# Optimization experiments

Hardware: AMD Instinct MI355X
Metric: run time of the kernel (lower is better)

## Reference

```python
import jax, jax.numpy as jnp
import numpy as np

N_SRC, N_DST, N_EDGE, D_IN, D_HID, D_OUT = 100000, 25000, 300000, 256, 256, 256


def setup_inputs() -> dict:
    key = jax.random.key(0)
    ks = jax.random.split(key, 9)
    # forward tensor args
    h_src = jax.random.normal(ks[0], (N_SRC, D_IN), dtype=jnp.float32)
    h_dst = jax.random.normal(ks[1], (N_DST, D_IN), dtype=jnp.float32)
    weights = jax.random.uniform(ks[2], (N_EDGE,), dtype=jnp.float32)
    src_idx = jax.random.randint(ks[3], (N_EDGE,), 0, N_SRC)
    dst_idx = jax.random.randint(ks[4], (N_EDGE,), 0, N_DST)
    # learned parameters (xavier_uniform with relu gain, zero bias)
    gain = float(np.sqrt(2.0))
    def xavier(k, fan_in, fan_out):
        a = gain * np.sqrt(6.0 / (fan_in + fan_out))
        return jax.random.uniform(k, (fan_in, fan_out), dtype=jnp.float32, minval=-a, maxval=a)
    Q_w = xavier(ks[5], D_IN, D_HID)            # stored [in, out]
    Q_b = jnp.zeros((D_HID,), dtype=jnp.float32)
    W_w = xavier(ks[6], D_IN + D_HID, D_OUT)    # stored [in, out]
    W_b = jnp.zeros((D_OUT,), dtype=jnp.float32)
    return {"h_src": h_src, "h_dst": h_dst, "weights": weights,
            "Q_w": Q_w, "Q_b": Q_b, "W_w": W_w, "W_b": W_b,
            "src_idx": src_idx, "dst_idx": dst_idx}


def reference(h_src, h_dst, weights, Q_w, Q_b, W_w, W_b, src_idx, dst_idx):
    n_dst = h_dst.shape[0]
    # nft = relu(Q(h_src))  (dropout is eval-mode identity)
    nft = jax.nn.relu(h_src @ Q_w + Q_b)                     # [N_src, H]
    # weighted neighbor sum: u_mul_e + sum over edges per dst node
    msg = nft[src_idx] * weights[:, None]                    # [E, H]
    n = jax.ops.segment_sum(msg, dst_idx, num_segments=n_dst)          # [N_dst, H]
    ws = jax.ops.segment_sum(weights, dst_idx, num_segments=n_dst)     # [N_dst]
    ws = jnp.clip(ws, 1.0, None)[:, None]
    z = jax.nn.relu(jnp.concatenate([n / ws, h_dst], axis=1) @ W_w + W_b)  # [N_dst, O]
    z_norm = jnp.linalg.norm(z, ord=2, axis=1, keepdims=True)
    z_norm = jnp.where(z_norm == 0, jnp.float32(1.0), z_norm)
    return z / z_norm
```

## Files before the change

kernel.cpp:

```cpp
#include <hip/hip_runtime.h>
#include <hip/hip_bf16.h>
#include <cstdint>

#define N_SRC 100000
#define N_DST 25000
#define N_EDGE 300000

typedef float f32x4 __attribute__((ext_vector_type(4)));
typedef __bf16 bf16x8 __attribute__((ext_vector_type(8)));

__device__ __forceinline__ unsigned short f2bf(float f) {
    union { float f; unsigned int u; } v; v.f = f;
    unsigned int u = v.u;
    u += 0x7FFFu + ((u >> 16) & 1u);
    return (unsigned short)(u >> 16);
}
__device__ __forceinline__ float bf2f(unsigned int bits16) {
    union { unsigned int u; float f; } v; v.u = bits16 << 16;
    return v.f;
}

__global__ void cast_weights(const float* __restrict__ Qw, const float* __restrict__ Ww,
                             unsigned short* __restrict__ Qt, unsigned short* __restrict__ Wt) {
    int i = blockIdx.x * blockDim.x + threadIdx.x;
    if (i < 256 * 256) {
        int n = i >> 8, k = i & 255;
        Qt[n * 256 + k] = f2bf(Qw[k * 256 + n]);
    } else if (i < 256 * 256 + 512 * 256) {
        int j = i - 256 * 256;
        int n = j >> 9, k = j & 511;
        Wt[n * 512 + k] = f2bf(Ww[k * 256 + n]);
    }
}

__global__ void hist_kernel(const int* __restrict__ dst_idx, int* __restrict__ counts) {
    int i = blockIdx.x * blockDim.x + threadIdx.x;
    if (i < N_EDGE) atomicAdd(&counts[dst_idx[i]], 1);
}

__global__ void scan_kernel(const int* __restrict__ counts, int* __restrict__ offsets, int n) {
    __shared__ int buf[1024];
    __shared__ int carry_s;
    int t = threadIdx.x;
    if (t == 0) { carry_s = 0; offsets[0] = 0; }
    __syncthreads();
    for (int base = 0; base < n; base += 1024) {
        int x = (base + t < n) ? counts[base + t] : 0;
        buf[t] = x;
        __syncthreads();
        for (int off = 1; off < 1024; off <<= 1) {
            int y = (t >= off) ? buf[t - off] : 0;
            __syncthreads();
            buf[t] += y;
            __syncthreads();
        }
        int incl = buf[t];
        int carry = carry_s;
        if (base + t < n) offsets[base + t + 1] = carry + incl;
        __syncthreads();
        if (t == 0) carry_s = carry + buf[1023];
        __syncthreads();
    }
}

__global__ void scatter_kernel(const int* __restrict__ dst_idx, const int* __restrict__ offsets,
                               int* __restrict__ cursor, int* __restrict__ edge_list) {
    int i = blockIdx.x * blockDim.x + threadIdx.x;
    if (i < N_EDGE) {
        int d = dst_idx[i];
        int pos = offsets[d] + atomicAdd(&cursor[d], 1);
        edge_list[pos] = i;
    }
}

template<int KDIM, bool A_BF16, bool NORM>
__global__ __launch_bounds__(256) void gemm_fused(
    const float* __restrict__ Af, const unsigned short* __restrict__ Ab,
    const unsigned short* __restrict__ Bt, const float* __restrict__ bias,
    unsigned short* __restrict__ Cb, float* __restrict__ Cf, int M)
{
    __shared__ __align__(16) unsigned short As[64 * 72];
    __shared__ __align__(16) unsigned short Bs[256 * 72];
    __shared__ float norml[4][64];

    const int tid = threadIdx.x;
    const int wave = tid >> 6, lane = tid & 63;
    const int g = lane >> 4, c = lane & 15;
    const int wn0 = wave * 64;
    const int m0 = blockIdx.x * 64;

    f32x4 acc[4][4];
    for (int i = 0; i < 4; ++i)
        for (int j = 0; j < 4; ++j)
            acc[i][j] = (f32x4){0.f, 0.f, 0.f, 0.f};

    for (int kt = 0; kt < KDIM / 64; ++kt) {
        const int k0 = kt * 64;
        if constexpr (A_BF16) {
            for (int i = 0; i < 2; ++i) {
                int idx = tid + i * 256;
                int row = idx >> 3, ch = idx & 7;
                int gm = m0 + row;
                uint4 v = {0u, 0u, 0u, 0u};
                if (gm < M) v = *reinterpret_cast<const uint4*>(Ab + (size_t)gm * KDIM + k0 + ch * 8);
                *reinterpret_cast<uint4*>(&As[row * 72 + ch * 8]) = v;
            }
        } else {
            for (int i = 0; i < 4; ++i) {
                int idx = tid + i * 256;
                int row = idx >> 4, f4 = idx & 15;
                int gm = m0 + row;
                float x0 = 0.f, x1 = 0.f, x2 = 0.f, x3 = 0.f;
                if (gm < M) {
                    const float4 v = *reinterpret_cast<const float4*>(Af + (size_t)gm * KDIM + k0 + f4 * 4);
                    x0 = v.x; x1 = v.y; x2 = v.z; x3 = v.w;
                }
                uint2 p;
                p.x = (unsigned)f2bf(x0) | ((unsigned)f2bf(x1) << 16);
                p.y = (unsigned)f2bf(x2) | ((unsigned)f2bf(x3) << 16);
                *reinterpret_cast<uint2*>(&As[row * 72 + f4 * 4]) = p;
            }
        }
        for (int i = 0; i < 8; ++i) {
            int idx = tid + i * 256;
            int n = idx >> 3, ch = idx & 7;
            uint4 v = *reinterpret_cast<const uint4*>(Bt + (size_t)n * KDIM + k0 + ch * 8);
            *reinterpret_cast<uint4*>(&Bs[n * 72 + ch * 8]) = v;
        }
        __syncthreads();
        for (int ks = 0; ks < 2; ++ks) {
            const int koff = ks * 32 + g * 8;
            bf16x8 a[4], b[4];
            for (int mi = 0; mi < 4; ++mi)
                a[mi] = *reinterpret_cast<const bf16x8*>(&As[(mi * 16 + c) * 72 + koff]);
            for (int ni = 0; ni < 4; ++ni)
                b[ni] = *reinterpret_cast<const bf16x8*>(&Bs[(wn0 + ni * 16 + c) * 72 + koff]);
            for (int mi = 0; mi < 4; ++mi)
                for (int ni = 0; ni < 4; ++ni)
                    acc[mi][ni] = __builtin_amdgcn_mfma_f32_16x16x32_bf16(a[mi], b[ni], acc[mi][ni], 0, 0, 0);
        }
        __syncthreads();
    }

    float bcol[4];
    for (int ni = 0; ni < 4; ++ni) bcol[ni] = bias[wn0 + ni * 16 + c];

    if constexpr (!NORM) {
        for (int mi = 0; mi < 4; ++mi) {
            int rowb = m0 + mi * 16 + g * 4;
            for (int ni = 0; ni < 4; ++ni) {
                int col = wn0 + ni * 16 + c;
                for (int r = 0; r < 4; ++r) {
                    int row = rowb + r;
                    if (row < M) {
                        float v = fmaxf(acc[mi][ni][r] + bcol[ni], 0.f);
                        Cb[(size_t)row * 256 + col] = f2bf(v);
                    }
                }
            }
        }
    } else {
        float ssq[4][4];
        for (int mi = 0; mi < 4; ++mi) {
            for (int r = 0; r < 4; ++r) {
                float s = 0.f;
                for (int ni = 0; ni < 4; ++ni) {
                    float v = fmaxf(acc[mi][ni][r] + bcol[ni], 0.f);
                    acc[mi][ni][r] = v;
                    s += v * v;
                }
                for (int m = 1; m < 16; m <<= 1) s += __shfl_xor(s, m, 64);
                ssq[mi][r] = s;
            }
        }
        if (c == 0) {
            for (int mi = 0; mi < 4; ++mi)
                for (int r = 0; r < 4; ++r)
                    norml[wave][mi * 16 + g * 4 + r] = ssq[mi][r];
        }
        __syncthreads();
        for (int mi = 0; mi < 4; ++mi) {
            int rowb = m0 + mi * 16 + g * 4;
            for (int r = 0; r < 4; ++r) {
                int rl = mi * 16 + g * 4 + r;
                float tot = norml[0][rl] + norml[1][rl] + norml[2][rl] + norml[3][rl];
                float rn = tot > 0.f ? rsqrtf(tot) : 1.0f;
                int row = rowb + r;
                if (row < M) {
                    for (int ni = 0; ni < 4; ++ni) {
                        int col = wn0 + ni * 16 + c;
                        Cf[(size_t)row * 256 + col] = acc[mi][ni][r] * rn;
                    }
                }
            }
        }
    }
}

__global__ __launch_bounds__(256) void aggregate_kernel(
    const unsigned short* __restrict__ nft, const float* __restrict__ h_dst,
    const float* __restrict__ weights, const int* __restrict__ src_idx,
    const int* __restrict__ edge_list, const int* __restrict__ offsets,
    unsigned short* __restrict__ xb)
{
    int d = blockIdx.x * 4 + (threadIdx.x >> 6);
    if (d >= N_DST) return;
    int lane = threadIdx.x & 63;
    int p0 = offsets[d], p1 = offsets[d + 1];
    float a0 = 0.f, a1 = 0.f, a2 = 0.f, a3 = 0.f, wsum = 0.f;
    for (int p = p0; p < p1; ++p) {
        int e = edge_list[p];
        float w = weights[e];
        int s = src_idx[e];
        wsum += w;
        uint2 v = *reinterpret_cast<const uint2*>(nft + (size_t)s * 256 + lane * 4);
        a0 += w * bf2f(v.x & 0xffffu);
        a1 += w * bf2f(v.x >> 16);
        a2 += w * bf2f(v.y & 0xffffu);
        a3 += w * bf2f(v.y >> 16);
    }
    float inv = 1.0f / fmaxf(wsum, 1.0f);
    uint2 p;
    p.x = (unsigned)f2bf(a0 * inv) | ((unsigned)f2bf(a1 * inv) << 16);
    p.y = (unsigned)f2bf(a2 * inv) | ((unsigned)f2bf(a3 * inv) << 16);
    *reinterpret_cast<uint2*>(xb + (size_t)d * 512 + lane * 4) = p;
    float4 h = *reinterpret_cast<const float4*>(h_dst + (size_t)d * 256 + lane * 4);
    uint2 q;
    q.x = (unsigned)f2bf(h.x) | ((unsigned)f2bf(h.y) << 16);
    q.y = (unsigned)f2bf(h.z) | ((unsigned)f2bf(h.w) << 16);
    *reinterpret_cast<uint2*>(xb + (size_t)d * 512 + 256 + lane * 4) = q;
}

extern "C" void kernel_launch(void* const* d_in, const int* in_sizes, int n_in,
                              void* d_out, int out_size, void* d_ws, size_t ws_size,
                              hipStream_t stream) {
    const float* h_src   = (const float*)d_in[0];
    const float* h_dst   = (const float*)d_in[1];
    const float* weights = (const float*)d_in[2];
    const float* Q_w     = (const float*)d_in[3];
    const float* Q_b     = (const float*)d_in[4];
    const float* W_w     = (const float*)d_in[5];
    const float* W_b     = (const float*)d_in[6];
    const int* src_idx   = (const int*)d_in[7];
    const int* dst_idx   = (const int*)d_in[8];
    float* out = (float*)d_out;

    char* ws = (char*)d_ws;
    unsigned short* nft = (unsigned short*)(ws);
    unsigned short* xb  = (unsigned short*)(ws + 51200000);
    unsigned short* Qt  = (unsigned short*)(ws + 76800000);
    unsigned short* Wt  = (unsigned short*)(ws + 76931072);
    int* counts    = (int*)(ws + 77193216);
    int* offsets   = (int*)(ws + 77293216);
    int* cursor    = (int*)(ws + 77393220);
    int* edge_list = (int*)(ws + 77493220);

    hipMemsetAsync(counts, 0, N_DST * sizeof(int), stream);
    hipMemsetAsync(cursor, 0, N_DST * sizeof(int), stream);

    cast_weights<<<768, 256, 0, stream>>>(Q_w, W_w, Qt, Wt);
    hist_kernel<<<(N_EDGE + 255) / 256, 256, 0, stream>>>(dst_idx, counts);
    scan_kernel<<<1, 1024, 0, stream>>>(counts, offsets, N_DST);
    scatter_kernel<<<(N_EDGE + 255) / 256, 256, 0, stream>>>(dst_idx, offsets, cursor, edge_list);

    gemm_fused<256, false, false><<<(N_SRC + 63) / 64, 256, 0, stream>>>(
        h_src, nullptr, Qt, Q_b, nft, nullptr, N_SRC);

    aggregate_kernel<<<N_DST / 4, 256, 0, stream>>>(
        nft, h_dst, weights, src_idx, edge_list, offsets, xb);

    gemm_fused<512, true, true><<<(N_DST + 63) / 64, 256, 0, stream>>>(
        nullptr, xb, Wt, W_b, nullptr, out, N_DST);

    (void)in_sizes; (void)n_in; (void)out_size; (void)ws_size;
}
```

Measured before the change: 233.8 us.

## Double-buffer GEMM A tiles, read B from global, wave-shuffle scan, unroll aggregation

Several unrelated changes land together. The GEMM drops the shared-memory B tile and loads B fragments straight from global memory into registers. It double-buffers the A tile in LDS with register prefetch and sets launch bounds to target two blocks per CU. The single-block scan switches from a shared-memory Hillis-Steele scan to wave shuffles, the scatter reuses the histogram counts via atomicSub so the cursor memset goes away, and the aggregation loop handles two edges per iteration to overlap the gathers. The main risks are B being reloaded from global by every block instead of staged in LDS, and register pressure from the B fragments and prefetch buffers.

Measured after the change: 188.8 us. 19.3% less time.

```diff
diff --git a/kernel.cpp b/kernel.cpp
--- a/kernel.cpp
+++ b/kernel.cpp
@@ -38,49 +38,58 @@
     if (i < N_EDGE) atomicAdd(&counts[dst_idx[i]], 1);
 }
 
-__global__ void scan_kernel(const int* __restrict__ counts, int* __restrict__ offsets, int n) {
-    __shared__ int buf[1024];
-    __shared__ int carry_s;
-    int t = threadIdx.x;
-    if (t == 0) { carry_s = 0; offsets[0] = 0; }
-    __syncthreads();
+__global__ __launch_bounds__(1024) void scan_kernel(const int* __restrict__ counts,
+                                                    int* __restrict__ offsets, int n) {
+    __shared__ int wsum[16];
+    const int t = threadIdx.x;
+    const int wid = t >> 6, lane = t & 63;
+    int carry = 0;
+    if (t == 0) offsets[0] = 0;
     for (int base = 0; base < n; base += 1024) {
         int x = (base + t < n) ? counts[base + t] : 0;
-        buf[t] = x;
-        __syncthreads();
-        for (int off = 1; off < 1024; off <<= 1) {
-            int y = (t >= off) ? buf[t - off] : 0;
-            __syncthreads();
-            buf[t] += y;
-            __syncthreads();
-        }
-        int incl = buf[t];
-        int carry = carry_s;
-        if (base + t < n) offsets[base + t + 1] = carry + incl;
-        __syncthreads();
-        if (t == 0) carry_s = carry + buf[1023];
+        #pragma unroll
+        for (int off = 1; off < 64; off <<= 1) {
+            int y = __shfl_up(x, off, 64);
+            if (lane >= off) x += y;
+        }
+        if (lane == 63) wsum[wid] = x;
+        __syncthreads();
+        if (t < 16) {
+            int w = wsum[t];
+            #pragma unroll
+            for (int off = 1; off < 16; off <<= 1) {
+                int y = __shfl_up(w, off, 64);
+                if (t >= off) w += y;
+            }
+            wsum[t] = w;
+        }
+        __syncthreads();
+        int pre = (wid > 0) ? wsum[wid - 1] : 0;
+        int incl = carry + pre + x;
+        if (base + t < n) offsets[base + t + 1] = incl;
+        carry += wsum[15];
         __syncthreads();
     }
 }
 
 __global__ void scatter_kernel(const int* __restrict__ dst_idx, const int* __restrict__ offsets,
-                               int* __restrict__ cursor, int* __restrict__ edge_list) {
+                               int* __restrict__ counts, int* __restrict__ edge_list) {
     int i = blockIdx.x * blockDim.x + threadIdx.x;
     if (i < N_EDGE) {
         int d = dst_idx[i];
-        int pos = offsets[d] + atomicAdd(&cursor[d], 1);
+        int pos = offsets[d] + (atomicSub(&counts[d], 1) - 1);
         edge_list[pos] = i;
     }
 }
 
 template<int KDIM, bool A_BF16, bool NORM>
-__global__ __launch_bounds__(256) void gemm_fused(
+__global__ __launch_bounds__(256, 2) void gemm_fused(
     const float* __restrict__ Af, const unsigned short* __restrict__ Ab,
     const unsigned short* __restrict__ Bt, const float* __restrict__ bias,
     unsigned short* __restrict__ Cb, float* __restrict__ Cf, int M)
 {
-    __shared__ __align__(16) unsigned short As[64 * 72];
-    __shared__ __align__(16) unsigned short Bs[256 * 72];
+    constexpr int NKT = KDIM / 64;
+    __shared__ __align__(16) unsigned short As[2][64 * 72];
     __shared__ float norml[4][64];
 
     const int tid = threadIdx.x;
@@ -90,66 +99,101 @@
     const int m0 = blockIdx.x * 64;
 
     f32x4 acc[4][4];
+    #pragma unroll
     for (int i = 0; i < 4; ++i)
+        #pragma unroll
         for (int j = 0; j < 4; ++j)
             acc[i][j] = (f32x4){0.f, 0.f, 0.f, 0.f};
 
-    for (int kt = 0; kt < KDIM / 64; ++kt) {
+    float4 sf[4];
+    uint4  sb[2];
+
+    auto issueA = [&](int kt) {
         const int k0 = kt * 64;
         if constexpr (A_BF16) {
+            #pragma unroll
             for (int i = 0; i < 2; ++i) {
                 int idx = tid + i * 256;
                 int row = idx >> 3, ch = idx & 7;
-                int gm = m0 + row;
-                uint4 v = {0u, 0u, 0u, 0u};
-                if (gm < M) v = *reinterpret_cast<const uint4*>(Ab + (size_t)gm * KDIM + k0 + ch * 8);
-                *reinterpret_cast<uint4*>(&As[row * 72 + ch * 8]) = v;
+                int gm = min(m0 + row, M - 1);
+                sb[i] = *reinterpret_cast<const uint4*>(Ab + (size_t)gm * KDIM + k0 + ch * 8);
             }
         } else {
+            #pragma unroll
             for (int i = 0; i < 4; ++i) {
                 int idx = tid + i * 256;
-                int row = idx >> 4, f4 = idx & 15;
-                int gm = m0 + row;
-                float x0 = 0.f, x1 = 0.f, x2 = 0.f, x3 = 0.f;
-                if (gm < M) {
-                    const float4 v = *reinterpret_cast<const float4*>(Af + (size_t)gm * KDIM + k0 + f4 * 4);
-                    x0 = v.x; x1 = v.y; x2 = v.z; x3 = v.w;
-                }
+                int row = idx >> 4, c4 = idx & 15;
+                int gm = min(m0 + row, M - 1);
+                sf[i] = *reinterpret_cast<const float4*>(Af + (size_t)gm * KDIM + k0 + c4 * 4);
+            }
+        }
+    };
+    auto writeA = [&](int buf) {
+        if constexpr (A_BF16) {
+            #pragma unroll
+            for (int i = 0; i < 2; ++i) {
+                int idx = tid + i * 256;
+                int row = idx >> 3, ch = idx & 7;
+                *reinterpret_cast<uint4*>(&As[buf][row * 72 + ch * 8]) = sb[i];
+            }
+        } else {
+            #pragma unroll
+            for (int i = 0; i < 4; ++i) {
+                int idx = tid + i * 256;
+                int row = idx >> 4, c4 = idx & 15;
                 uint2 p;
-                p.x = (unsigned)f2bf(x0) | ((unsigned)f2bf(x1) << 16);
-                p.y = (unsigned)f2bf(x2) | ((unsigned)f2bf(x3) << 16);
-                *reinterpret_cast<uint2*>(&As[row * 72 + f4 * 4]) = p;
-            }
-        }
-        for (int i = 0; i < 8; ++i) {
-            int idx = tid + i * 256;
-            int n = idx >> 3, ch = idx & 7;
-            uint4 v = *reinterpret_cast<const uint4*>(Bt + (size_t)n * KDIM + k0 + ch * 8);
-            *reinterpret_cast<uint4*>(&Bs[n * 72 + ch * 8]) = v;
-        }
-        __syncthreads();
+                p.x = (unsigned)f2bf(sf[i].x) | ((unsigned)f2bf(sf[i].y) << 16);
+                p.y = (unsigned)f2bf(sf[i].z) | ((unsigned)f2bf(sf[i].w) << 16);
+                *reinterpret_cast<uint2*>(&As[buf][row * 72 + c4 * 4]) = p;
+            }
+        }
+    };
+
+    issueA(0);
+    writeA(0);
+    __syncthreads();
+
+    #pragma unroll
+    for (int kt = 0; kt < NKT; ++kt) {
+        const int cur = kt & 1;
+        if (kt + 1 < NKT) issueA(kt + 1);
+        const int k0 = kt * 64;
+        bf16x8 bfrag[2][4];
+        #pragma unroll
+        for (int ks = 0; ks < 2; ++ks)
+            #pragma unroll
+            for (int ni = 0; ni < 4; ++ni)
+                bfrag[ks][ni] = *reinterpret_cast<const bf16x8*>(
+                    Bt + (size_t)(wn0 + ni * 16 + c) * KDIM + k0 + ks * 32 + g * 8);
+        #pragma unroll
         for (int ks = 0; ks < 2; ++ks) {
             const int koff = ks * 32 + g * 8;
-            bf16x8 a[4], b[4];
+            bf16x8 a[4];
+            #pragma unroll
             for (int mi = 0; mi < 4; ++mi)
-                a[mi] = *reinterpret_cast<const bf16x8*>(&As[(mi * 16 + c) * 72 + koff]);
-            for (int ni = 0; ni < 4; ++ni)
-                b[ni] = *reinterpret_cast<const bf16x8*>(&Bs[(wn0 + ni * 16 + c) * 72 + koff]);
+                a[mi] = *reinterpret_cast<const bf16x8*>(&As[cur][(mi * 16 + c) * 72 + koff]);
+            #pragma unroll
             for (int mi = 0; mi < 4; ++mi)
+                #pragma unroll
                 for (int ni = 0; ni < 4; ++ni)
-                    acc[mi][ni] = __builtin_amdgcn_mfma_f32_16x16x32_bf16(a[mi], b[ni], acc[mi][ni], 0, 0, 0);
-        }
+                    acc[mi][ni] = __builtin_amdgcn_mfma_f32_16x16x32_bf16(a[mi], bfrag[ks][ni], acc[mi][ni], 0, 0, 0);
+        }
+        if (kt + 1 < NKT) writeA(cur ^ 1);
         __syncthreads();
     }
 
     float bcol[4];
+    #pragma unroll
     for (int ni = 0; ni < 4; ++ni) bcol[ni] = bias[wn0 + ni * 16 + c];
 
     if constexpr (!NORM) {
+        #pragma unroll
         for (int mi = 0; mi < 4; ++mi) {
             int rowb = m0 + mi * 16 + g * 4;
+            #pragma unroll
             for (int ni = 0; ni < 4; ++ni) {
                 int col = wn0 + ni * 16 + c;
+                #pragma unroll
                 for (int r = 0; r < 4; ++r) {
                     int row = rowb + r;
                     if (row < M) {
@@ -161,32 +205,41 @@
         }
     } else {
         float ssq[4][4];
+        #pragma unroll
         for (int mi = 0; mi < 4; ++mi) {
+            #pragma unroll
             for (int r = 0; r < 4; ++r) {
                 float s = 0.f;
+                #pragma unroll
                 for (int ni = 0; ni < 4; ++ni) {
                     float v = fmaxf(acc[mi][ni][r] + bcol[ni], 0.f);
                     acc[mi][ni][r] = v;
                     s += v * v;
                 }
+                #pragma unroll
                 for (int m = 1; m < 16; m <<= 1) s += __shfl_xor(s, m, 64);
                 ssq[mi][r] = s;
             }
         }
         if (c == 0) {
+            #pragma unroll
             for (int mi = 0; mi < 4; ++mi)
+                #pragma unroll
                 for (int r = 0; r < 4; ++r)
                     norml[wave][mi * 16 + g * 4 + r] = ssq[mi][r];
         }
         __syncthreads();
+        #pragma unroll
         for (int mi = 0; mi < 4; ++mi) {
             int rowb = m0 + mi * 16 + g * 4;
+            #pragma unroll
             for (int r = 0; r < 4; ++r) {
                 int rl = mi * 16 + g * 4 + r;
                 float tot = norml[0][rl] + norml[1][rl] + norml[2][rl] + norml[3][rl];
                 float rn = tot > 0.f ? rsqrtf(tot) : 1.0f;
                 int row = rowb + r;
                 if (row < M) {
+                    #pragma unroll
                     for (int ni = 0; ni < 4; ++ni) {
                         int col = wn0 + ni * 16 + c;
                         Cf[(size_t)row * 256 + col] = acc[mi][ni][r] * rn;
@@ -208,7 +261,20 @@
     int lane = threadIdx.x & 63;
     int p0 = offsets[d], p1 = offsets[d + 1];
     float a0 = 0.f, a1 = 0.f, a2 = 0.f, a3 = 0.f, wsum = 0.f;
-    for (int p = p0; p < p1; ++p) {
+    int p = p0;
+    for (; p + 1 < p1; p += 2) {
+        int e0 = edge_list[p], e1 = edge_list[p + 1];
+        float w0 = weights[e0], w1 = weights[e1];
+        int s0 = src_idx[e0], s1 = src_idx[e1];
+        uint2 v0 = *reinterpret_cast<const uint2*>(nft + (size_t)s0 * 256 + lane * 4);
+        uint2 v1 = *reinterpret_cast<const uint2*>(nft + (size_t)s1 * 256 + lane * 4);
+        wsum += w0 + w1;
+        a0 += w0 * bf2f(v0.x & 0xffffu) + w1 * bf2f(v1.x & 0xffffu);
+        a1 += w0 * bf2f(v0.x >> 16)     + w1 * bf2f(v1.x >> 16);
+        a2 += w0 * bf2f(v0.y & 0xffffu) + w1 * bf2f(v1.y & 0xffffu);
+        a3 += w0 * bf2f(v0.y >> 16)     + w1 * bf2f(v1.y >> 16);
+    }
+    if (p < p1) {
         int e = edge_list[p];
         float w = weights[e];
         int s = src_idx[e];
@@ -220,10 +286,10 @@
         a3 += w * bf2f(v.y >> 16);
     }
     float inv = 1.0f / fmaxf(wsum, 1.0f);
-    uint2 p;
-    p.x = (unsigned)f2bf(a0 * inv) | ((unsigned)f2bf(a1 * inv) << 16);
-    p.y = (unsigned)f2bf(a2 * inv) | ((unsigned)f2bf(a3 * inv) << 16);
-    *reinterpret_cast<uint2*>(xb + (size_t)d * 512 + lane * 4) = p;
+    uint2 pk;
+    pk.x = (unsigned)f2bf(a0 * inv) | ((unsigned)f2bf(a1 * inv) << 16);
+    pk.y = (unsigned)f2bf(a2 * inv) | ((unsigned)f2bf(a3 * inv) << 16);
+    *reinterpret_cast<uint2*>(xb + (size_t)d * 512 + lane * 4) = pk;
     float4 h = *reinterpret_cast<const float4*>(h_dst + (size_t)d * 256 + lane * 4);
     uint2 q;
     q.x = (unsigned)f2bf(h.x) | ((unsigned)f2bf(h.y) << 16);
@@ -252,16 +318,14 @@
     unsigned short* Wt  = (unsigned short*)(ws + 76931072);
     int* counts    = (int*)(ws + 77193216);
     int* offsets   = (int*)(ws + 77293216);
-    int* cursor    = (int*)(ws + 77393220);
-    int* edge_list = (int*)(ws + 77493220);
+    int* edge_list = (int*)(ws + 77393220);
 
     hipMemsetAsync(counts, 0, N_DST * sizeof(int), stream);
-    hipMemsetAsync(cursor, 0, N_DST * sizeof(int), stream);
 
     cast_weights<<<768, 256, 0, stream>>>(Q_w, W_w, Qt, Wt);
     hist_kernel<<<(N_EDGE + 255) / 256, 256, 0, stream>>>(dst_idx, counts);
     scan_kernel<<<1, 1024, 0, stream>>>(counts, offsets, N_DST);
-    scatter_kernel<<<(N_EDGE + 255) / 256, 256, 0, stream>>>(dst_idx, offsets, cursor, edge_list);
+    scatter_kernel<<<(N_EDGE + 255) / 256, 256, 0, stream>>>(dst_idx, offsets, counts, edge_list);
 
     gemm_fused<256, false, false><<<(N_SRC + 63) / 64, 256, 0, stream>>>(
         h_src, nullptr, Qt, Q_b, nft, nullptr, N_SRC);
```
